# Optimization experiments

Hardware: AMD Instinct MI355X
Metric: run time of the kernel (lower is better)

The kernel has to match this reference:

```python
import jax, jax.numpy as jnp
import numpy as np

NUM_CLASSES = 128


def setup_inputs() -> dict:
    key = jax.random.key(0)
    k1, k2, k3 = jax.random.split(key, 3)
    B, T, C = 64, 2048, NUM_CLASSES
    emissions = jax.random.normal(k1, (B, T, C), dtype=jnp.float32)
    tags = jax.random.randint(k2, (B, T), 0, C, dtype=jnp.int32)
    # learned params (glorot-ish scale for transitions, zeros for start/end)
    transitions = jax.random.normal(k3, (C, C), dtype=jnp.float32) * 0.1
    start_transitions = jnp.zeros((C,), dtype=jnp.float32)
    end_transitions = jnp.zeros((C,), dtype=jnp.float32)
    return {
        "emissions": emissions,
        "tags": tags,
        "transitions": transitions,
        "start_transitions": start_transitions,
        "end_transitions": end_transitions,
    }


def _log_partition(emissions, trans, start, end):
    # forward algorithm: sequential logsumexp-add semiring scan over T
    alpha0 = start + emissions[:, 0]                      # (B, C)
    em_rest = jnp.swapaxes(emissions[:, 1:], 0, 1)        # (T-1, B, C)

    def step(alpha, emit):
        scores = alpha[:, :, None] + trans[None]          # (B, C_from, C_to)
        alpha = jax.nn.logsumexp(scores, axis=1) + emit   # (B, C)
        return alpha, None

    alpha, _ = jax.lax.scan(step, alpha0, em_rest)
    return jax.nn.logsumexp(alpha + end, axis=-1)         # (B,)


def _gold_score(emissions, tags, trans, start, end):
    emit_total = jnp.take_along_axis(emissions, tags[:, :, None], axis=2)[:, :, 0].sum(-1)  # (B,)
    trans_total = trans[tags[:, :-1], tags[:, 1:]].sum(-1)                                  # (B,)
    return start[tags[:, 0]] + emit_total + trans_total + end[tags[:, -1]]


def _viterbi(emissions, trans, start, end):
    v0 = start + emissions[:, 0]                          # (B, C)
    em_rest = jnp.swapaxes(emissions[:, 1:], 0, 1)        # (T-1, B, C)

    def step(v, emit):
        scores = v[:, :, None] + trans[None]              # (B, C_from, C_to)
        best_from = jnp.argmax(scores, axis=1).astype(jnp.int32)  # (B, C)
        v = jnp.max(scores, axis=1) + emit
        return v, best_from

    v, bps = jax.lax.scan(step, v0, em_rest)              # bps: (T-1, B, C)
    v = v + end
    best_last = jnp.argmax(v, axis=-1).astype(jnp.int32)  # (B,)

    def back(best, bp):
        best = jnp.take_along_axis(bp, best[:, None], axis=1)[:, 0]
        return best, best

    _, path_rev = jax.lax.scan(back, best_last, bps, reverse=True)  # (T-1, B)
    paths = jnp.concatenate([path_rev, best_last[None]], axis=0)    # (T, B)
    return paths.T                                                   # (B, T)


def reference(emissions, tags, transitions, start_transitions, end_transitions):
    trans, start, end = transitions, start_transitions, end_transitions
    # CRF NLL (training loss path): log Z - gold path score
    log_Z = _log_partition(emissions, trans, start, end)
    gold = _gold_score(emissions, tags, trans, start, end)
    nll = log_Z - gold                                    # (B,)
    # inference path: one-hot Viterbi decode, as in call(training=False)
    paths = _viterbi(emissions, trans, start, end)        # (B, T)
    onehot = jax.nn.one_hot(paths, NUM_CLASSES, dtype=emissions.dtype)  # (B, T, C)
    return nll, onehot
```

## Files before the change

kernel.cpp:

```cpp
#include <hip/hip_runtime.h>
#include <stdint.h>

#define NB 64
#define NT 2048
#define NC 128
#define KF 32
#define LF 64
#define WF 8
#define NVB 256
#define KV 16
#define LV 128
#define WV 32

typedef _Float16 h2 __attribute__((ext_vector_type(2)));

__device__ __forceinline__ h2 bc2(uint32_t u) { return __builtin_bit_cast(h2, u); }

__device__ __forceinline__ float fdot2f(h2 a, h2 b, float c) {
#if __has_builtin(__builtin_amdgcn_fdot2)
  return __builtin_amdgcn_fdot2(a, b, c, false);
#else
  float d;
  asm("v_dot2_f32_f16 %0, %1, %2, %3"
      : "=v"(d)
      : "v"(__builtin_bit_cast(uint32_t, a)), "v"(__builtin_bit_cast(uint32_t, b)), "v"(c));
  return d;
#endif
}

#define DPP_FMAX_STAGE(vv, ctrl)                                               \
  {                                                                            \
    int t_ = __builtin_amdgcn_update_dpp(vv, vv, ctrl, 0xf, 0xf, false);       \
    vv = __builtin_bit_cast(int, fmaxf(__builtin_bit_cast(float, vv),          \
                                       __builtin_bit_cast(float, t_)));        \
  }

__device__ __forceinline__ float wave_max_bcast(float x) {
  int v = __builtin_bit_cast(int, x);
  DPP_FMAX_STAGE(v, 0x111);
  DPP_FMAX_STAGE(v, 0x112);
  DPP_FMAX_STAGE(v, 0x114);
  DPP_FMAX_STAGE(v, 0x118);
  DPP_FMAX_STAGE(v, 0x142);
  DPP_FMAX_STAGE(v, 0x143);
  return __builtin_bit_cast(float, __builtin_amdgcn_readlane(v, 63));
}

__device__ __forceinline__ float readlanef(float v, int l) {
  return __builtin_bit_cast(float, __builtin_amdgcn_readlane(__builtin_bit_cast(int, v), l));
}

__device__ __forceinline__ int mbcnt64(unsigned long long m) {
  return __builtin_amdgcn_mbcnt_hi((uint32_t)(m >> 32),
                                   __builtin_amdgcn_mbcnt_lo((uint32_t)m, 0));
}

__device__ __forceinline__ size_t slot_off(int b, int t) {
  return ((size_t)64 + ((size_t)b * NT + t) * NC) * 4;
}

union ScanSM {
  float itr[64 * 256];
  uint32_t ea[4][2][64];
};

__global__ __launch_bounds__(256, 1) void scan_kernel(
    const float* __restrict__ em, const float* __restrict__ trans,
    const float* __restrict__ startv, const float* __restrict__ endv,
    float* __restrict__ out, float* __restrict__ fpart, int* __restrict__ best_last) {
  __shared__ __align__(16) ScanSM sm;
  const int lane = threadIdx.x & 63;
  const int wid = threadIdx.x >> 6;

  if (blockIdx.x >= NVB) {
    const int fi = (blockIdx.x - NVB) * 4 + wid;
    const int b = fi >> 5, c = fi & 31;
    const int t0 = (c == 0) ? 0 : c * LF - WF;
    const int tend = (c == KF - 1) ? (NT - 1) : (c + 1) * LF;
    const float* emb = em + (size_t)b * NT * NC;

    h2 e0[64], e1[64];
#pragma unroll
    for (int j = 0; j < 64; ++j) {
      float2 r0 = *(const float2*)(trans + (size_t)(2 * j) * NC + 2 * lane);
      float2 r1 = *(const float2*)(trans + (size_t)(2 * j + 1) * NC + 2 * lane);
      h2 a, bb;
      a.x = (_Float16)__expf(r0.x);  a.y = (_Float16)__expf(r1.x);
      bb.x = (_Float16)__expf(r0.y); bb.y = (_Float16)__expf(r1.y);
      e0[j] = a; e1[j] = bb;
    }
    float2 ev = *(const float2*)(endv + 2 * lane);
    float2 em0 = *(const float2*)(emb + (size_t)t0 * NC + 2 * lane);
    float2 nx0 = *(const float2*)(emb + (size_t)(t0 + 1) * NC + 2 * lane);
    float2 nx1 = *(const float2*)(emb + (size_t)(t0 + 2) * NC + 2 * lane);
    float2 nx2 = *(const float2*)(emb + (size_t)(t0 + 3) * NC + 2 * lane);
    float2 nx3 = *(const float2*)(emb + (size_t)(t0 + 4) * NC + 2 * lane);
    float u0 = em0.x, u1 = em0.y;
    if (c == 0) {
      float2 sv = *(const float2*)(startv + 2 * lane);
      u0 += sv.x; u1 += sv.y;
    }
    float mu = 0.f;
    uint32_t* eab0 = &sm.ea[wid][0][0];
    uint32_t* eab1 = &sm.ea[wid][1][0];

    auto fstep = [&](int t, float2& nx) {
      h2 eh; eh.x = (_Float16)__expf(u0); eh.y = (_Float16)__expf(u1);
      uint32_t* eab = (t & 1) ? eab1 : eab0;
      eab[lane] = __builtin_bit_cast(uint32_t, eh);
      float nm = wave_max_bcast(fmaxf(u0, u1));
      asm volatile("s_waitcnt lgkmcnt(0)" ::: "memory");
      float A0 = 0.f, A1 = 0.f, A2 = 0.f, A3 = 0.f;
#pragma unroll
      for (int q = 0; q < 16; ++q) {
        uint4 w = *(const uint4*)&eab[q * 4];
        A0 = fdot2f(bc2(w.x), e0[4 * q + 0], A0); A1 = fdot2f(bc2(w.x), e1[4 * q + 0], A1);
        A2 = fdot2f(bc2(w.y), e0[4 * q + 1], A2); A3 = fdot2f(bc2(w.y), e1[4 * q + 1], A3);
        A0 = fdot2f(bc2(w.z), e0[4 * q + 2], A0); A1 = fdot2f(bc2(w.z), e1[4 * q + 2], A1);
        A2 = fdot2f(bc2(w.w), e0[4 * q + 3], A2); A3 = fdot2f(bc2(w.w), e1[4 * q + 3], A3);
      }
      float o0 = nx.x - nm, o1 = nx.y - nm;
      u0 = __logf(A0 + A2) + o0;
      u1 = __logf(A1 + A3) + o1;
      mu += nm;
      if (t + 4 <= tend) nx = *(const float2*)(emb + (size_t)(t + 4) * NC + 2 * lane);
    };

    auto wave_lse = [&](float x0, float x1) -> float {
      float m = wave_max_bcast(fmaxf(x0, x1));
      float ss = __expf(x0 - m) + __expf(x1 - m);
#pragma unroll
      for (int s = 1; s < 64; s <<= 1) ss += __shfl_xor(ss, s, 64);
      return m + __logf(ss);
    };

    int t = t0 + 1;
    float m_start = 0.f;
    if (c > 0) {
      for (int j = 0; j < WF / 4; ++j) {
        fstep(t, nx0); fstep(t + 1, nx1); fstep(t + 2, nx2); fstep(t + 3, nx3);
        t += 4;
      }
      m_start = mu + wave_lse(u0, u1);
    }
    for (; t + 3 <= tend; t += 4) {
      fstep(t, nx0); fstep(t + 1, nx1); fstep(t + 2, nx2); fstep(t + 3, nx3);
    }
    int rem = tend - t + 1;
    if (rem > 0) fstep(t, nx0);
    if (rem > 1) fstep(t + 1, nx1);
    if (rem > 2) fstep(t + 2, nx2);

    float m_end;
    if (c == KF - 1) m_end = mu + wave_lse(u0 + ev.x, u1 + ev.y);
    else             m_end = mu + wave_lse(u0, u1);
    if (lane == 0) fpart[b * KF + c] = m_end - m_start;
  } else {
    const int fi = blockIdx.x * 4 + wid;
    const int b = fi >> 4, c = fi & 15;
    const float* emb = em + (size_t)b * NT * NC;
    char* ob = (char*)out;
    for (int r = wid * 32; r < wid * 32 + 32; ++r) {
      float2 w = *(const float2*)(trans + (size_t)r * NC + 2 * lane);
      int l = r >> 1, p = r & 1;
      sm.itr[l * 256 + (2 * lane) * 2 + p] = w.x;
      sm.itr[l * 256 + (2 * lane + 1) * 2 + p] = w.y;
    }
    __syncthreads();
    float rmx0 = -INFINITY, rmn0 = INFINITY, rmx1 = -INFINITY, rmn1 = INFINITY;
    for (int j = 0; j < 64; ++j) {
      int jj = (j + lane) & 63;
      float4 q = *(const float4*)&sm.itr[lane * 256 + jj * 4];
      rmx0 = fmaxf(rmx0, fmaxf(q.x, q.z)); rmn0 = fminf(rmn0, fminf(q.x, q.z));
      rmx1 = fmaxf(rmx1, fmaxf(q.y, q.w)); rmn1 = fminf(rmn1, fminf(q.y, q.w));
    }

    const int trec = c * LV;
    const int tend = trec + LV;
    float2 ev = *(const float2*)(endv + 2 * lane);
    float v0, v1;
    int t;
    if (c == 0) {
      float2 sv = *(const float2*)(startv + 2 * lane);
      float2 em0 = *(const float2*)(emb + 2 * lane);
      v0 = sv.x + em0.x; v1 = sv.y + em0.y;
      t = 1;
    } else {
      int t0 = trec - 1 - WV;
      float2 em0 = *(const float2*)(emb + (size_t)t0 * NC + 2 * lane);
      v0 = em0.x; v1 = em0.y;
      t = t0 + 1;
    }
    float2 nx0 = *(const float2*)(emb + (size_t)t * NC + 2 * lane);
    float2 nx1 = *(const float2*)(emb + (size_t)(t + 1) * NC + 2 * lane);
    float2 nx2 = *(const float2*)(emb + (size_t)(t + 2) * NC + 2 * lane);
    float2 nx3 = *(const float2*)(emb + (size_t)(t + 3) * NC + 2 * lane);
    const float4* itb = (const float4*)&sm.itr[4 * lane];

    auto cmax = [&](int l, float4 q, float& c0, float& c1) {
      float ve = readlanef(v0, l);
      float vo = readlanef(v1, l);
      c0 = fmaxf(ve + q.x, vo + q.y);
      c1 = fmaxf(ve + q.z, vo + q.w);
    };

    auto wstep = [&](int tt, float2& nx) {
      float thr = wave_max_bcast(fmaxf(v0 + rmn0, v1 + rmn1));
      unsigned long long m0 = __ballot(v0 + rmx0 >= thr);
      unsigned long long m1 = __ballot(v1 + rmx1 >= thr);
      unsigned long long r = m0 | m1;
      if (!r) r = 1ull;
      float best0, best1;
      {
        int l0 = (int)__builtin_ctzll(r); r &= r - 1;
        int l1 = r ? (int)__builtin_ctzll(r) : l0; r = r ? (r & (r - 1)) : 0ull;
        int l2 = r ? (int)__builtin_ctzll(r) : l0; r = r ? (r & (r - 1)) : 0ull;
        int l3 = r ? (int)__builtin_ctzll(r) : l0; r = r ? (r & (r - 1)) : 0ull;
        float4 q0 = itb[l0 * 64], q1 = itb[l1 * 64], q2 = itb[l2 * 64], q3 = itb[l3 * 64];
        float a0, a1, b0c, b1c, c0c, c1c, d0c, d1c;
        cmax(l0, q0, a0, a1); cmax(l1, q1, b0c, b1c);
        cmax(l2, q2, c0c, c1c); cmax(l3, q3, d0c, d1c);
        best0 = fmaxf(fmaxf(a0, b0c), fmaxf(c0c, d0c));
        best1 = fmaxf(fmaxf(a1, b1c), fmaxf(c1c, d1c));
        while (r) {
          int la = (int)__builtin_ctzll(r); r &= r - 1;
          int lb = r ? (int)__builtin_ctzll(r) : la; r = r ? (r & (r - 1)) : 0ull;
          int lc = r ? (int)__builtin_ctzll(r) : la; r = r ? (r & (r - 1)) : 0ull;
          int ld = r ? (int)__builtin_ctzll(r) : la; r = r ? (r & (r - 1)) : 0ull;
          float4 qa = itb[la * 64], qb = itb[lb * 64], qc = itb[lc * 64], qd = itb[ld * 64];
          float x0, x1, y0, y1, z0, z1, w0, w1;
          cmax(la, qa, x0, x1); cmax(lb, qb, y0, y1);
          cmax(lc, qc, z0, z1); cmax(ld, qd, w0, w1);
          best0 = fmaxf(best0, fmaxf(fmaxf(x0, y0), fmaxf(z0, w0)));
          best1 = fmaxf(best1, fmaxf(fmaxf(x1, y1), fmaxf(z1, w1)));
        }
      }
      v0 = best0 + nx.x; v1 = best1 + nx.y;
      if (tt + 4 < NT) nx = *(const float2*)(emb + (size_t)(tt + 4) * NC + 2 * lane);
    };

    auto vstep = [&](int tt, float2& nx) {
      float thr = wave_max_bcast(fmaxf(v0 + rmn0, v1 + rmn1));
      unsigned long long m0 = __ballot(v0 + rmx0 >= thr);
      unsigned long long m1 = __ballot(v1 + rmx1 >= thr);
      unsigned long long rem = m0 | m1;
      if (!rem) rem = 1ull;
      int cnt = (int)__popcll(rem);
      int nvals = (int)__popcll(m0) + (int)__popcll(m1);
      char* rec = ob + slot_off(b, tt);
      float best0, best1;

      if (__builtin_expect(nvals <= 92, 1)) {
        if (lane == 0) {
          *(unsigned long long*)(rec + 128) = m0;
          *(unsigned long long*)(rec + 136) = m1;
        }
        int plt = mbcnt64(m0) + mbcnt64(m1);
        int hasE = (int)((m0 >> lane) & 1ull);
        if (hasE) *(float*)(rec + 144 + 4 * plt) = v0;
        if ((m1 >> lane) & 1ull) *(float*)(rec + 144 + 4 * (plt + hasE)) = v1;
        unsigned long long r = rem;
        if (__builtin_expect(cnt <= 4, 1)) {
          int l0 = (int)__builtin_ctzll(r); r &= r - 1;
          int l1 = r ? (int)__builtin_ctzll(r) : l0; r = r ? (r & (r - 1)) : 0ull;
          int l2 = r ? (int)__builtin_ctzll(r) : l0; r = r ? (r & (r - 1)) : 0ull;
          int l3 = r ? (int)__builtin_ctzll(r) : l0; r = r ? (r & (r - 1)) : 0ull;
          float4 q0 = itb[l0 * 64], q1 = itb[l1 * 64], q2 = itb[l2 * 64], q3 = itb[l3 * 64];
          float a0, a1, b0c, b1c, c0c, c1c, d0c, d1c;
          cmax(l0, q0, a0, a1); cmax(l1, q1, b0c, b1c);
          cmax(l2, q2, c0c, c1c); cmax(l3, q3, d0c, d1c);
          best0 = fmaxf(fmaxf(a0, b0c), fmaxf(c0c, d0c));
          best1 = fmaxf(fmaxf(a1, b1c), fmaxf(c1c, d1c));
        } else {
          int l0 = (int)__builtin_ctzll(r); r &= r - 1;
          int l1 = r ? (int)__builtin_ctzll(r) : l0; r = r ? (r & (r - 1)) : 0ull;
          int l2 = r ? (int)__builtin_ctzll(r) : l0; r = r ? (r & (r - 1)) : 0ull;
          int l3 = r ? (int)__builtin_ctzll(r) : l0; r = r ? (r & (r - 1)) : 0ull;
          int l4 = r ? (int)__builtin_ctzll(r) : l0; r = r ? (r & (r - 1)) : 0ull;
          int l5 = r ? (int)__builtin_ctzll(r) : l0; r = r ? (r & (r - 1)) : 0ull;
          int l6 = r ? (int)__builtin_ctzll(r) : l0; r = r ? (r & (r - 1)) : 0ull;
          int l7 = r ? (int)__builtin_ctzll(r) : l0; r = r ? (r & (r - 1)) : 0ull;
          float4 q0 = itb[l0 * 64], q1 = itb[l1 * 64], q2 = itb[l2 * 64], q3 = itb[l3 * 64];
          float4 q4 = itb[l4 * 64], q5 = itb[l5 * 64], q6 = itb[l6 * 64], q7 = itb[l7 * 64];
          float a0, a1, b0c, b1c, c0c, c1c, d0c, d1c;
          float e0c, e1c, f0c, f1c, g0c, g1c, h0c, h1c;
          cmax(l0, q0, a0, a1); cmax(l1, q1, b0c, b1c);
          cmax(l2, q2, c0c, c1c); cmax(l3, q3, d0c, d1c);
          cmax(l4, q4, e0c, e1c); cmax(l5, q5, f0c, f1c);
          cmax(l6, q6, g0c, g1c); cmax(l7, q7, h0c, h1c);
          best0 = fmaxf(fmaxf(fmaxf(a0, b0c), fmaxf(c0c, d0c)),
                        fmaxf(fmaxf(e0c, f0c), fmaxf(g0c, h0c)));
          best1 = fmaxf(fmaxf(fmaxf(a1, b1c), fmaxf(c1c, d1c)),
                        fmaxf(fmaxf(e1c, f1c), fmaxf(g1c, h1c)));
          while (r) {
            int la = (int)__builtin_ctzll(r); r &= r - 1;
            int lb = r ? (int)__builtin_ctzll(r) : la; r = r ? (r & (r - 1)) : 0ull;
            int lc = r ? (int)__builtin_ctzll(r) : la; r = r ? (r & (r - 1)) : 0ull;
            int ld = r ? (int)__builtin_ctzll(r) : la; r = r ? (r & (r - 1)) : 0ull;
            float4 qa = itb[la * 64], qb = itb[lb * 64], qc = itb[lc * 64], qd = itb[ld * 64];
            float x0, x1, y0, y1, z0, z1, w0, w1;
            cmax(la, qa, x0, x1); cmax(lb, qb, y0, y1);
            cmax(lc, qc, z0, z1); cmax(ld, qd, w0, w1);
            best0 = fmaxf(best0, fmaxf(fmaxf(x0, y0), fmaxf(z0, w0)));
            best1 = fmaxf(best1, fmaxf(fmaxf(x1, y1), fmaxf(z1, w1)));
          }
        }
      } else {
        if (lane == 0) {
          *(unsigned long long*)(rec + 128) = 0ull;
          *(unsigned long long*)(rec + 136) = 0ull;
        }
        best0 = -INFINITY; best1 = -INFINITY;
        int bi0 = 0, bi1 = 0;
        unsigned long long r = rem;
        do {
          int l0 = (int)__builtin_ctzll(r); r &= r - 1;
          int l1 = l0, l2 = l0, l3 = l0;
          if (r) {
            l1 = (int)__builtin_ctzll(r); r &= r - 1;
            if (r) {
              l2 = (int)__builtin_ctzll(r); r &= r - 1;
              if (r) { l3 = (int)__builtin_ctzll(r); r &= r - 1; }
            }
          }
          float4 q0 = itb[l0 * 64], q1 = itb[l1 * 64], q2 = itb[l2 * 64], q3 = itb[l3 * 64];
          auto proc = [&](int lc, float4 q) {
            if ((m0 >> lc) & 1ull) {
              float vce = readlanef(v0, lc);
              float s0 = vce + q.x, s1 = vce + q.z;
              bool g0 = s0 > best0; best0 = g0 ? s0 : best0; bi0 = g0 ? 2 * lc : bi0;
              bool g1 = s1 > best1; best1 = g1 ? s1 : best1; bi1 = g1 ? 2 * lc : bi1;
            }
            if ((m1 >> lc) & 1ull) {
              float vco = readlanef(v1, lc);
              float s0 = vco + q.y, s1 = vco + q.w;
              bool g0 = s0 > best0; best0 = g0 ? s0 : best0; bi0 = g0 ? 2 * lc + 1 : bi0;
              bool g1 = s1 > best1; best1 = g1 ? s1 : best1; bi1 = g1 ? 2 * lc + 1 : bi1;
            }
          };
          proc(l0, q0); proc(l1, q1); proc(l2, q2); proc(l3, q3);
        } while (r);
        *(uint16_t*)(rec + 2 * lane) = (uint16_t)((bi0 & 0xff) | (bi1 << 8));
      }

      v0 = best0 + nx.x; v1 = best1 + nx.y;
      if (tt + 4 < NT) nx = *(const float2*)(emb + (size_t)(tt + 4) * NC + 2 * lane);
    };

    if (c > 0) {
      for (int k = 0; k < WV / 4; ++k) {
        wstep(t, nx0); wstep(t + 1, nx1); wstep(t + 2, nx2); wstep(t + 3, nx3);
        t += 4;
      }
    }
    for (; t + 3 < tend; t += 4) {
      vstep(t, nx0); vstep(t + 1, nx1); vstep(t + 2, nx2); vstep(t + 3, nx3);
    }
    if (t < tend) vstep(t, nx0);
    if (t + 1 < tend) vstep(t + 1, nx1);
    if (t + 2 < tend) vstep(t + 2, nx2);

    if (c == KV - 1) {
      v0 += ev.x; v1 += ev.y;
      float bv = v0; int bix = 2 * lane;
      if (v1 > bv) { bv = v1; bix = 2 * lane + 1; }
#pragma unroll
      for (int s = 1; s < 64; s <<= 1) {
        float ovv = __shfl_xor(bv, s, 64);
        int oi = __shfl_xor(bix, s, 64);
        if (ovv > bv || (ovv == bv && oi < bix)) { bv = ovv; bix = oi; }
      }
      if (lane == 0) best_last[b] = bix;
    }
  }
}

__global__ __launch_bounds__(128) void bp_kernel(const float* __restrict__ trans,
                                                 float* __restrict__ out) {
  int bid = blockIdx.x, b = bid >> 5, cc = bid & 31, ct = threadIdx.x;
  char* ob = (char*)out;
  int lo = cc * 64, hi = cc * 64 + 63;
  if (lo < 1) lo = 1;
  for (int t = lo; t <= hi; ++t) {
    char* rec = ob + slot_off(b, t);
    unsigned long long m0 = *(const unsigned long long*)(rec + 128);
    unsigned long long m1 = *(const unsigned long long*)(rec + 136);
    unsigned long long rem = m0 | m1;
    if (rem == 0ull) continue;
    const float* vals = (const float*)(rec + 144);
    float best = -INFINITY;
    int bi = 0, idx = 0;
    do {
      int l = (int)__builtin_ctzll(rem); rem &= rem - 1;
      if ((m0 >> l) & 1ull) {
        float s = vals[idx++] + trans[(size_t)(2 * l) * NC + ct];
        if (s > best) { best = s; bi = 2 * l; }
      }
      if ((m1 >> l) & 1ull) {
        float s = vals[idx++] + trans[(size_t)(2 * l + 1) * NC + ct];
        if (s > best) { best = s; bi = 2 * l + 1; }
      }
    } while (rem);
    ((uint8_t*)rec)[ct] = (uint8_t)bi;
  }
}

__global__ __launch_bounds__(512) void maps_kernel(
    const float* __restrict__ out, uint8_t* __restrict__ mmap,
    uint8_t* __restrict__ tmap, const float* __restrict__ em,
    const int* __restrict__ tags, const float* __restrict__ trans,
    const float* __restrict__ startv, const float* __restrict__ endv,
    const float* __restrict__ fpart, float* __restrict__ outw) {
  __shared__ uint8_t bp[256 * 128];
  __shared__ uint8_t G[4][128];
  __shared__ float red[512];
  int tid = threadIdx.x;
  if (blockIdx.x >= 512) {
    int b = blockIdx.x - 512;
    const float* emb = em + (size_t)b * NT * NC;
    const int* tgb = tags + (size_t)b * NT;
    float acc = 0.f;
    for (int j = 0; j < NT / 512; ++j) {
      int t = tid + j * 512;
      int tg = tgb[t];
      acc += emb[(size_t)t * NC + tg];
      if (t < NT - 1) acc += trans[(size_t)tg * NC + tgb[t + 1]];
    }
    red[tid] = acc;
    __syncthreads();
    for (int s = 256; s > 0; s >>= 1) {
      if (tid < s) red[tid] += red[tid + s];
      __syncthreads();
    }
    if (tid == 0) {
      float z = 0.f;
      for (int c = 0; c < KF; ++c) z += fpart[b * KF + c];
      outw[b] = z - (red[0] + startv[tgb[0]] + endv[tgb[NT - 1]]);
    }
    return;
  }
  int bid = blockIdx.x, b = bid >> 3, c = bid & 7;
  const char* ob = (const char*)out;
  int lo_t = c * 256 + 1;
  int nrows = (c == 7) ? 255 : 256;
  int nd = nrows * 32;
  for (int k = 0; k < 16; ++k) {
    int d = tid + k * 512;
    if (d < nd) {
      int row = d >> 5, col = d & 31;
      *(uint32_t*)&bp[(size_t)d * 4] =
          *(const uint32_t*)(ob + slot_off(b, lo_t + row) + (size_t)col * 4);
    }
  }
  __syncthreads();
  int g = tid >> 7, s = tid & 127;
  int glo = g * 64;
  int ghi = glo + 64; if (ghi > nrows) ghi = nrows;
  int cur = s;
  for (int i = ghi - 1; i >= glo; --i) cur = bp[i * 128 + cur];
  G[g][s] = (uint8_t)cur;
  __syncthreads();
  if (tid < 128) {
    int x = G[3][tid]; x = G[2][x]; x = G[1][x]; x = G[0][x];
    mmap[b * 1024 + c * 128 + tid] = (uint8_t)x;
    if (c < 7) tmap[b * 1024 + c * 128 + tid] = bp[255 * 128 + tid];
  }
}

__global__ __launch_bounds__(512) void replay_kernel(float* __restrict__ out,
                                                     const uint8_t* __restrict__ mmap,
                                                     const uint8_t* __restrict__ tmap,
                                                     const int* __restrict__ best_last) {
  __shared__ uint8_t bp[255 * 128];
  __shared__ uint8_t G[3][128];
  __shared__ uint8_t path[256];
  int bid = blockIdx.x, b = bid >> 3, c = bid & 7, tid = threadIdx.x;
  char* ob = (char*)out;
  int lo_t = c * 256 + 1;
  const int nd = 255 * 32;
  for (int k = 0; k < 16; ++k) {
    int d = tid + k * 512;
    if (d < nd) {
      int row = d >> 5, col = d & 31;
      *(uint32_t*)&bp[(size_t)d * 4] =
          *(const uint32_t*)(ob + slot_off(b, lo_t + row) + (size_t)col * 4);
    }
  }
  __syncthreads();
  if (tid < 384) {
    int g = tid >> 7, s = tid & 127;
    int glo = 64 + g * 64;
    int ghi = glo + 64; if (ghi > 255) ghi = 255;
    int cur = s;
    for (int i = ghi - 1; i >= glo; --i) cur = bp[i * 128 + cur];
    G[g][s] = (uint8_t)cur;
  }
  __syncthreads();
  if (tid < 4) {
    int e = best_last[b];
    for (int cc = 7; cc > c; --cc) e = mmap[b * 1024 + cc * 128 + e];
    int top = (c == 7) ? best_last[b] : tmap[b * 1024 + c * 128 + e];
    int w = tid;
    int seed, hi;
    if (w == 3) { seed = top; hi = 254; path[255] = (uint8_t)top; }
    else {
      int x = G[2][top];
      if (w <= 1) x = G[1][x];
      if (w == 0) x = G[0][x];
      seed = x; hi = w * 64 + 63;
    }
    int cur = seed;
    for (int i = hi; i >= w * 64; --i) { cur = bp[i * 128 + cur]; path[i] = (uint8_t)cur; }
  }
  __syncthreads();
  for (int k = 0; k < 16; ++k) {
    int idx = tid + k * 512;
    int row = idx >> 5, j = idx & 31;
    int p = path[row];
    int c0 = j * 4;
    float4 val;
    val.x = (c0 + 0 == p) ? 1.f : 0.f;
    val.y = (c0 + 1 == p) ? 1.f : 0.f;
    val.z = (c0 + 2 == p) ? 1.f : 0.f;
    val.w = (c0 + 3 == p) ? 1.f : 0.f;
    *(float4*)(ob + slot_off(b, c * 256 + row) + (size_t)j * 16) = val;
  }
}

extern "C" void kernel_launch(void* const* d_in, const int* in_sizes, int n_in,
                              void* d_out, int out_size, void* d_ws, size_t ws_size,
                              hipStream_t stream) {
  const float* em = (const float*)d_in[0];
  const int* tags = (const int*)d_in[1];
  const float* trans = (const float*)d_in[2];
  const float* startv = (const float*)d_in[3];
  const float* endv = (const float*)d_in[4];
  float* out = (float*)d_out;
  char* ws = (char*)d_ws;
  float* fpart = (float*)(ws + 0);
  int* best_last = (int*)(ws + 8192);
  uint8_t* mmap = (uint8_t*)(ws + 9216);
  uint8_t* tmap = (uint8_t*)(ws + 9216 + 65536);

  scan_kernel<<<dim3(NVB + 512), dim3(256), 0, stream>>>(em, trans, startv, endv, out,
                                                         fpart, best_last);
  bp_kernel<<<dim3(2048), dim3(128), 0, stream>>>(trans, out);
  maps_kernel<<<dim3(512 + 64), dim3(512), 0, stream>>>(out, mmap, tmap, em, tags,
                                                        trans, startv, endv, fpart, out);
  replay_kernel<<<dim3(512), dim3(512), 0, stream>>>(out, mmap, tmap, best_last);
}
```

Baseline: 304.4 us.

## Store Viterbi transition tile as fp16 in LDS and halve warmup window

The transition matrix kept in shared memory for the Viterbi blocks is now stored as fp16, read as 4-half vectors and widened to float. This halves LDS footprint and per-lookup bandwidth but adds conversion instructions and rounds the transition scores, which can change argmax ties and decoded paths. Separately, the Viterbi chunk warmup window WV drops from 32 to 16 steps, cutting redundant recomputation at the cost of a higher risk that chunk boundaries have not converged to the true path.

```diff
diff --git a/kernel.cpp b/kernel.cpp
--- a/kernel.cpp
+++ b/kernel.cpp
@@ -10,11 +10,16 @@
 #define NVB 256
 #define KV 16
 #define LV 128
-#define WV 32
+#define WV 16
 
 typedef _Float16 h2 __attribute__((ext_vector_type(2)));
+typedef _Float16 h4 __attribute__((ext_vector_type(4)));
 
 __device__ __forceinline__ h2 bc2(uint32_t u) { return __builtin_bit_cast(h2, u); }
+
+__device__ __forceinline__ float4 h4f(h4 a) {
+  return make_float4((float)a.x, (float)a.y, (float)a.z, (float)a.w);
+}
 
 __device__ __forceinline__ float fdot2f(h2 a, h2 b, float c) {
 #if __has_builtin(__builtin_amdgcn_fdot2)
@@ -60,7 +65,7 @@
 }
 
 union ScanSM {
-  float itr[64 * 256];
+  _Float16 itr[64 * 256];
   uint32_t ea[4][2][64];
 };
 
@@ -163,14 +168,14 @@
     for (int r = wid * 32; r < wid * 32 + 32; ++r) {
       float2 w = *(const float2*)(trans + (size_t)r * NC + 2 * lane);
       int l = r >> 1, p = r & 1;
-      sm.itr[l * 256 + (2 * lane) * 2 + p] = w.x;
-      sm.itr[l * 256 + (2 * lane + 1) * 2 + p] = w.y;
+      sm.itr[l * 256 + (2 * lane) * 2 + p] = (_Float16)w.x;
+      sm.itr[l * 256 + (2 * lane + 1) * 2 + p] = (_Float16)w.y;
     }
     __syncthreads();
     float rmx0 = -INFINITY, rmn0 = INFINITY, rmx1 = -INFINITY, rmn1 = INFINITY;
     for (int j = 0; j < 64; ++j) {
       int jj = (j + lane) & 63;
-      float4 q = *(const float4*)&sm.itr[lane * 256 + jj * 4];
+      float4 q = h4f(*(const h4*)&sm.itr[lane * 256 + jj * 4]);
       rmx0 = fmaxf(rmx0, fmaxf(q.x, q.z)); rmn0 = fminf(rmn0, fminf(q.x, q.z));
       rmx1 = fmaxf(rmx1, fmaxf(q.y, q.w)); rmn1 = fminf(rmn1, fminf(q.y, q.w));
     }
@@ -195,7 +200,7 @@
     float2 nx1 = *(const float2*)(emb + (size_t)(t + 1) * NC + 2 * lane);
     float2 nx2 = *(const float2*)(emb + (size_t)(t + 2) * NC + 2 * lane);
     float2 nx3 = *(const float2*)(emb + (size_t)(t + 3) * NC + 2 * lane);
-    const float4* itb = (const float4*)&sm.itr[4 * lane];
+    const h4* itb = (const h4*)&sm.itr[4 * lane];
 
     auto cmax = [&](int l, float4 q, float& c0, float& c1) {
       float ve = readlanef(v0, l);
@@ -216,7 +221,8 @@
         int l1 = r ? (int)__builtin_ctzll(r) : l0; r = r ? (r & (r - 1)) : 0ull;
         int l2 = r ? (int)__builtin_ctzll(r) : l0; r = r ? (r & (r - 1)) : 0ull;
         int l3 = r ? (int)__builtin_ctzll(r) : l0; r = r ? (r & (r - 1)) : 0ull;
-        float4 q0 = itb[l0 * 64], q1 = itb[l1 * 64], q2 = itb[l2 * 64], q3 = itb[l3 * 64];
+        float4 q0 = h4f(itb[l0 * 64]), q1 = h4f(itb[l1 * 64]);
+        float4 q2 = h4f(itb[l2 * 64]), q3 = h4f(itb[l3 * 64]);
         float a0, a1, b0c, b1c, c0c, c1c, d0c, d1c;
         cmax(l0, q0, a0, a1); cmax(l1, q1, b0c, b1c);
         cmax(l2, q2, c0c, c1c); cmax(l3, q3, d0c, d1c);
@@ -227,7 +233,8 @@
           int lb = r ? (int)__builtin_ctzll(r) : la; r = r ? (r & (r - 1)) : 0ull;
           int lc = r ? (int)__builtin_ctzll(r) : la; r = r ? (r & (r - 1)) : 0ull;
           int ld = r ? (int)__builtin_ctzll(r) : la; r = r ? (r & (r - 1)) : 0ull;
-          float4 qa = itb[la * 64], qb = itb[lb * 64], qc = itb[lc * 64], qd = itb[ld * 64];
+          float4 qa = h4f(itb[la * 64]), qb = h4f(itb[lb * 64]);
+          float4 qc = h4f(itb[lc * 64]), qd = h4f(itb[ld * 64]);
           float x0, x1, y0, y1, z0, z1, w0, w1;
           cmax(la, qa, x0, x1); cmax(lb, qb, y0, y1);
           cmax(lc, qc, z0, z1); cmax(ld, qd, w0, w1);
@@ -265,7 +272,8 @@
           int l1 = r ? (int)__builtin_ctzll(r) : l0; r = r ? (r & (r - 1)) : 0ull;
           int l2 = r ? (int)__builtin_ctzll(r) : l0; r = r ? (r & (r - 1)) : 0ull;
           int l3 = r ? (int)__builtin_ctzll(r) : l0; r = r ? (r & (r - 1)) : 0ull;
-          float4 q0 = itb[l0 * 64], q1 = itb[l1 * 64], q2 = itb[l2 * 64], q3 = itb[l3 * 64];
+          float4 q0 = h4f(itb[l0 * 64]), q1 = h4f(itb[l1 * 64]);
+          float4 q2 = h4f(itb[l2 * 64]), q3 = h4f(itb[l3 * 64]);
           float a0, a1, b0c, b1c, c0c, c1c, d0c, d1c;
           cmax(l0, q0, a0, a1); cmax(l1, q1, b0c, b1c);
           cmax(l2, q2, c0c, c1c); cmax(l3, q3, d0c, d1c);
@@ -280,8 +288,10 @@
           int l5 = r ? (int)__builtin_ctzll(r) : l0; r = r ? (r & (r - 1)) : 0ull;
           int l6 = r ? (int)__builtin_ctzll(r) : l0; r = r ? (r & (r - 1)) : 0ull;
           int l7 = r ? (int)__builtin_ctzll(r) : l0; r = r ? (r & (r - 1)) : 0ull;
-          float4 q0 = itb[l0 * 64], q1 = itb[l1 * 64], q2 = itb[l2 * 64], q3 = itb[l3 * 64];
-          float4 q4 = itb[l4 * 64], q5 = itb[l5 * 64], q6 = itb[l6 * 64], q7 = itb[l7 * 64];
+          float4 q0 = h4f(itb[l0 * 64]), q1 = h4f(itb[l1 * 64]);
+          float4 q2 = h4f(itb[l2 * 64]), q3 = h4f(itb[l3 * 64]);
+          float4 q4 = h4f(itb[l4 * 64]), q5 = h4f(itb[l5 * 64]);
+          float4 q6 = h4f(itb[l6 * 64]), q7 = h4f(itb[l7 * 64]);
           float a0, a1, b0c, b1c, c0c, c1c, d0c, d1c;
           float e0c, e1c, f0c, f1c, g0c, g1c, h0c, h1c;
           cmax(l0, q0, a0, a1); cmax(l1, q1, b0c, b1c);
@@ -297,7 +307,8 @@
             int lb = r ? (int)__builtin_ctzll(r) : la; r = r ? (r & (r - 1)) : 0ull;
             int lc = r ? (int)__builtin_ctzll(r) : la; r = r ? (r & (r - 1)) : 0ull;
             int ld = r ? (int)__builtin_ctzll(r) : la; r = r ? (r & (r - 1)) : 0ull;
-            float4 qa = itb[la * 64], qb = itb[lb * 64], qc = itb[lc * 64], qd = itb[ld * 64];
+            float4 qa = h4f(itb[la * 64]), qb = h4f(itb[lb * 64]);
+            float4 qc = h4f(itb[lc * 64]), qd = h4f(itb[ld * 64]);
             float x0, x1, y0, y1, z0, z1, w0, w1;
             cmax(la, qa, x0, x1); cmax(lb, qb, y0, y1);
             cmax(lc, qc, z0, z1); cmax(ld, qd, w0, w1);
@@ -323,7 +334,8 @@
               if (r) { l3 = (int)__builtin_ctzll(r); r &= r - 1; }
             }
           }
-          float4 q0 = itb[l0 * 64], q1 = itb[l1 * 64], q2 = itb[l2 * 64], q3 = itb[l3 * 64];
+          float4 q0 = h4f(itb[l0 * 64]), q1 = h4f(itb[l1 * 64]);
+          float4 q2 = h4f(itb[l2 * 64]), q3 = h4f(itb[l3 * 64]);
           auto proc = [&](int lc, float4 q) {
             if ((m0 >> lc) & 1ull) {
               float vce = readlanef(v0, lc);
```

Measured after the change: 306.2 us, median of 2. No clear change (+0.6%).
